# Kernel optimization log

Measured on AMD Instinct MI355X. Metric: run time of the kernel, lower is better.

## Reference

```python
import jax, jax.numpy as jnp
import numpy as np

K = 10        # neighbors kept (after dropping self)
N_SEEDS = 20  # FPS seeds
H = 0.01      # repulsion bandwidth


def setup_inputs() -> dict:
    key = jax.random.key(0)
    pcs = jax.random.uniform(key, (16, 65536, 3), dtype=jnp.float32)
    return {"pcs": pcs}


def farthest_point_sample(xyz, npoint, key):
    """Iterative FPS. xyz: [B,N,C] -> centroids [B,npoint] (int)."""
    B, N, C = xyz.shape
    distance = jnp.full((B, N), 1e10, dtype=xyz.dtype)
    farthest = jax.random.randint(key, (B,), 0, N)
    bidx = jnp.arange(B)

    def step(carry, _):
        dist_min, far = carry
        centroid = xyz[bidx, far][:, None, :]              # [B,1,C]
        d = jnp.sum((xyz - centroid) ** 2, axis=-1)        # [B,N]
        dist_min = jnp.minimum(dist_min, d)
        return (dist_min, jnp.argmax(dist_min, axis=-1)), far

    _, cents = jax.lax.scan(step, (distance, farthest), None, length=npoint)
    return cents.T  # [B, npoint]


def reference(pcs):
    B, N, C = pcs.shape
    seeds = farthest_point_sample(pcs, N_SEEDS, jax.random.key(1))   # [B,S]
    seeds_value = jnp.take_along_axis(
        pcs, jnp.broadcast_to(seeds[:, :, None], (B, N_SEEDS, C)), axis=1
    )  # [B,S,3]
    diff = pcs[:, :, None, :] - seeds_value[:, None, :, :]           # [B,N,S,3]
    sq = jnp.sum(diff * diff, axis=-1)                               # [B,N,S]
    # safe L2 norm (exact zeros at seed-vs-itself)
    dist = jnp.where(sq == 0, 0.0, jnp.sqrt(jnp.where(sq == 0, 1.0, sq)))
    dist_sn = dist.transpose(0, 2, 1)                                # [B,S,N]
    # k+1 smallest distances per seed, ascending (torch.topk largest=False)
    neg_top, _ = jax.lax.top_k(-dist_sn, K + 1)                      # [B,S,K+1]
    top_dist_net = -neg_top[:, :, 1:]                                # drop self, [B,S,K]
    weights = jnp.exp(-(top_dist_net ** 2) / (H * H))
    repulsion = -top_dist_net * weights
    return repulsion.sum(axis=2).sum(axis=1).mean()
```

## Files before the change

kernel.cpp:

```cpp
#include <hip/hip_runtime.h>
#include <cstdint>
#include <cfloat>
#include <cmath>

#define NPTS 65536
#define NB 16
#define NS 20
#define KK 10
#define FPB 16
#define NSm1 (NS - 1)

struct InitIdx { int idx[NB]; };

static __device__ __forceinline__ unsigned long long
agent_ld(const unsigned long long* p) {
    return __hip_atomic_load(p, __ATOMIC_RELAXED, __HIP_MEMORY_SCOPE_AGENT);
}
static __device__ __forceinline__ unsigned int
agent_ld32(const unsigned int* p) {
    return __hip_atomic_load(p, __ATOMIC_RELAXED, __HIP_MEMORY_SCOPE_AGENT);
}

#define INS11(L, SQ)                                                     \
    {                                                                    \
        _Pragma("unroll")                                                \
        for (int jj = 10; jj >= 1; --jj)                                 \
            L[jj] = __builtin_amdgcn_fmed3f(L[jj - 1], L[jj], (SQ));     \
        L[0] = fminf(L[0], (SQ));                                        \
    }

__global__ __launch_bounds__(1024, 4) void fps_kernel(const float* __restrict__ pcs,
                                                      unsigned long long* __restrict__ fkey,
                                                      unsigned int* __restrict__ part,
                                                      float* __restrict__ out,
                                                      InitIdx init) {
    const int u   = blockIdx.x;
    const int xcd = u & 7;
    const int k   = u >> 3;
    const int b   = 2 * xcd + (k >> 4);
    const int j   = k & 15;
    const int t   = threadIdx.x;
    const int lane = t & 63;
    const int w    = t >> 6;
    const float* __restrict__ base = pcs + (size_t)b * NPTS * 3;
    const int pbase = j * 4096 + t * 4;

    const float4* q4 = reinterpret_cast<const float4*>(base + (size_t)pbase * 3);
    float4 A = q4[0], Bv = q4[1], Cv = q4[2];
    float x[4] = { A.x, A.w, Bv.z, Cv.y };
    float y[4] = { A.y, Bv.x, Bv.w, Cv.z };
    float z[4] = { A.z, Bv.y, Cv.x, Cv.w };
    float dm[4] = { 1e10f, 1e10f, 1e10f, 1e10f };

    __shared__ float s_val[16];
    __shared__ int   s_idx[16];
    __shared__ int   s_far;
    __shared__ int   s_seeds[NS];
    __shared__ float xs[4096];
    __shared__ float ys[4096];
    __shared__ float zs[4096];

    int far = init.idx[b];

    for (int s = 0; s < NS; ++s) {
        if (t == 0) s_seeds[s] = far;
        if (s == NSm1) break;

        const float* c = base + (size_t)far * 3;
        const float cx = c[0], cy = c[1], cz = c[2];

        float bestv = -1.0f;
        int   besti = 0;
#pragma unroll
        for (int q = 0; q < 4; ++q) {
            float dx = __fsub_rn(x[q], cx);
            float dy = __fsub_rn(y[q], cy);
            float dz = __fsub_rn(z[q], cz);
            float d  = __fadd_rn(__fadd_rn(__fmul_rn(dx, dx), __fmul_rn(dy, dy)),
                                 __fmul_rn(dz, dz));
            dm[q] = fminf(dm[q], d);
            if (dm[q] > bestv) { bestv = dm[q]; besti = pbase + q; }
        }
#pragma unroll
        for (int off = 32; off >= 1; off >>= 1) {
            float ov = __shfl_down(bestv, off);
            int   oi = __shfl_down(besti, off);
            if (ov > bestv || (ov == bestv && oi < besti)) { bestv = ov; besti = oi; }
        }
        if (lane == 0) { s_val[w] = bestv; s_idx[w] = besti; }
        __syncthreads();

        if (w == 0) {
            unsigned long long kv = 0ULL;
            if (lane < 16) {
                kv = ((unsigned long long)__float_as_uint(s_val[lane]) << 32) |
                     (unsigned long long)(0xFFFFFFFFu - (unsigned int)s_idx[lane]);
            }
#pragma unroll
            for (int off = 8; off >= 1; off >>= 1) {
                unsigned int lo = (unsigned int)kv, hi = (unsigned int)(kv >> 32);
                unsigned int olo = (unsigned int)__shfl_xor((int)lo, off);
                unsigned int ohi = (unsigned int)__shfl_xor((int)hi, off);
                unsigned long long o = ((unsigned long long)ohi << 32) | olo;
                if (o > kv) kv = o;
            }
            unsigned long long* fp = fkey + (size_t)(b * NS + s) * FPB;
            if (lane == 0)
                __hip_atomic_store(&fp[j], kv, __ATOMIC_RELAXED,
                                   __HIP_MEMORY_SCOPE_AGENT);

            const unsigned long long* sl = fp + (lane & 15);
            unsigned long long p0 = agent_ld(sl);
            unsigned long long p1 = agent_ld(sl);
            unsigned long long p2 = agent_ld(sl);
            unsigned long long v;
            for (;;) {
                if (!__any(p0 == 0ULL)) { v = p0; break; }
                p0 = agent_ld(sl);
                if (!__any(p1 == 0ULL)) { v = p1; break; }
                p1 = agent_ld(sl);
                if (!__any(p2 == 0ULL)) { v = p2; break; }
                p2 = agent_ld(sl);
            }
#pragma unroll
            for (int off = 32; off >= 1; off >>= 1) {
                unsigned int lo = (unsigned int)v, hi = (unsigned int)(v >> 32);
                unsigned int olo = (unsigned int)__shfl_xor((int)lo, off);
                unsigned int ohi = (unsigned int)__shfl_xor((int)hi, off);
                unsigned long long o = ((unsigned long long)ohi << 32) | olo;
                if (o > v) v = o;
            }
            if (lane == 0)
                s_far = (int)(0xFFFFFFFFu - (unsigned int)(v & 0xFFFFFFFFull));
        }
        __syncthreads();
        far = s_far;
    }

    {
        float4* xv = reinterpret_cast<float4*>(xs);
        float4* yv = reinterpret_cast<float4*>(ys);
        float4* zv = reinterpret_cast<float4*>(zs);
        xv[t] = make_float4(x[0], x[1], x[2], x[3]);
        yv[t] = make_float4(y[0], y[1], y[2], y[3]);
        zv[t] = make_float4(z[0], z[1], z[2], z[3]);
    }
    __syncthreads();

#pragma unroll
    for (int pass = 0; pass < 2; ++pass) {
        const int s2 = w + pass * 16;
        if (s2 >= NS) break;
        const int sidx = s_seeds[s2];
        const float ccx = base[(size_t)sidx * 3 + 0];
        const float ccy = base[(size_t)sidx * 3 + 1];
        const float ccz = base[(size_t)sidx * 3 + 2];

        float lst[11];
#pragma unroll
        for (int jj = 0; jj < 11; ++jj) lst[jj] = FLT_MAX;

        const float4* xv = reinterpret_cast<const float4*>(xs);
        const float4* yv = reinterpret_cast<const float4*>(ys);
        const float4* zv = reinterpret_cast<const float4*>(zs);
        for (int i = 0; i < 16; ++i) {
            const int p4 = i * 64 + lane;
            float4 qx = xv[p4], qy = yv[p4], qz = zv[p4];
            float px[4] = { qx.x, qx.y, qx.z, qx.w };
            float py[4] = { qy.x, qy.y, qy.z, qy.w };
            float pz[4] = { qz.x, qz.y, qz.z, qz.w };
#pragma unroll
            for (int q = 0; q < 4; ++q) {
                float dx = __fsub_rn(px[q], ccx);
                float dy = __fsub_rn(py[q], ccy);
                float dz = __fsub_rn(pz[q], ccz);
                float sq = __fadd_rn(__fadd_rn(__fmul_rn(dx, dx), __fmul_rn(dy, dy)),
                                     __fmul_rn(dz, dz));
                INS11(lst, sq);
            }
        }
        unsigned int* pr = part + ((size_t)(b * NS + s2) * FPB + j) * 11;
        for (int r = 0; r < 11; ++r) {
            float v = lst[0];
#pragma unroll
            for (int off = 32; off >= 1; off >>= 1) v = fminf(v, __shfl_xor(v, off));
            unsigned long long m = __ballot(lst[0] == v);
            if (lane == (int)__ffsll(m) - 1) {
#pragma unroll
                for (int jj = 0; jj < 10; ++jj) lst[jj] = lst[jj + 1];
                lst[10] = FLT_MAX;
            }
            if (lane == 0)
                __hip_atomic_store(&pr[r], __float_as_uint(v) + 1u,
                                   __ATOMIC_RELAXED, __HIP_MEMORY_SCOPE_AGENT);
        }
    }

    for (int s2 = j; s2 < NS; s2 += FPB) {
        if (w == 0) {
            const unsigned int* sl2 = part + (size_t)(b * NS + s2) * FPB * 11;
            unsigned int k0 = 0, k1 = 0, k2 = (lane + 128 < 176) ? 0u : 1u;
            do {
                if (k0 == 0) k0 = agent_ld32(&sl2[lane]);
                if (k1 == 0) k1 = agent_ld32(&sl2[lane + 64]);
                if (k2 == 0) k2 = agent_ld32(&sl2[lane + 128]);
            } while (__any(k0 == 0 || k1 == 0 || k2 == 0));
            float a0 = __uint_as_float(k0 - 1u);
            float a1 = __uint_as_float(k1 - 1u);
            float a2 = (lane + 128 < 176) ? __uint_as_float(k2 - 1u) : FLT_MAX;

            const float HH = (float)(0.01 * 0.01);
            float acc = 0.0f;
#pragma unroll
            for (int r = 0; r < 11; ++r) {
                float mymin = fminf(a0, fminf(a1, a2));
                float v = mymin;
#pragma unroll
                for (int off = 32; off >= 1; off >>= 1) v = fminf(v, __shfl_xor(v, off));
                unsigned long long m = __ballot(mymin == v);
                if (lane == (int)__ffsll(m) - 1) {
                    if (a0 == v)      a0 = FLT_MAX;
                    else if (a1 == v) a1 = FLT_MAX;
                    else              a2 = FLT_MAX;
                }
                if (lane == 0 && r >= 1) {
                    float sq = v;
                    float dd = (sq == 0.0f) ? 0.0f : __fsqrt_rn(sq);
                    float q2 = __fmul_rn(dd, dd);
                    float wt = expf(__fdiv_rn(-q2, HH));
                    acc = __fadd_rn(acc, -__fmul_rn(dd, wt));
                }
            }
            if (lane == 0) atomicAdd(out, acc * 0.0625f);
        }
    }
}

static inline uint32_t rotl32(uint32_t x, uint32_t d) { return (x << d) | (x >> (32 - d)); }

static void tf2x32(uint32_t k0, uint32_t k1, uint32_t x0, uint32_t x1,
                   uint32_t& y0, uint32_t& y1) {
    const uint32_t ks[3] = { k0, k1, k0 ^ k1 ^ 0x1BD11BDAu };
    const uint32_t rotA[4] = { 13, 15, 26, 6 };
    const uint32_t rotB[4] = { 17, 29, 16, 24 };
    uint32_t v0 = x0 + ks[0], v1 = x1 + ks[1];
    for (int i = 0; i < 5; ++i) {
        const uint32_t* rot = (i % 2 == 0) ? rotA : rotB;
        for (int j = 0; j < 4; ++j) {
            v0 += v1;
            v1 = rotl32(v1, rot[j]);
            v1 ^= v0;
        }
        v0 += ks[(i + 1) % 3];
        v1 += ks[(i + 2) % 3] + (uint32_t)(i + 1);
    }
    y0 = v0; y1 = v1;
}

extern "C" void kernel_launch(void* const* d_in, const int* in_sizes, int n_in,
                              void* d_out, int out_size, void* d_ws, size_t ws_size,
                              hipStream_t stream) {
    const float* pcs = (const float*)d_in[0];
    float* out = (float*)d_out;

    unsigned long long* fkey = (unsigned long long*)((char*)d_ws + 2048);
    unsigned int* part       = (unsigned int*)((char*)d_ws + 49152);

    uint32_t k2_0, k2_1;
    tf2x32(0u, 1u, 0u, 1u, k2_0, k2_1);
    InitIdx init;
    for (int i = 0; i < NB; ++i) {
        uint32_t y0, y1;
        tf2x32(k2_0, k2_1, 0u, (uint32_t)i, y0, y1);
        init.idx[i] = (int)((y0 ^ y1) & 0xFFFFu);
    }

    hipMemsetAsync((char*)d_ws + 2048, 0, 272384, stream);
    hipMemsetAsync(d_out, 0, sizeof(float), stream);

    hipLaunchKernelGGL(fps_kernel, dim3(NB * FPB), dim3(1024), 0, stream,
                       pcs, fkey, part, out, init);
}
```

Baseline: 73.00 us.

## Overlap per-seed kNN scan with FPS global reduction using idle warps

The per-seed nearest-neighbour scan now runs inside the FPS loop. Warp 0 does the cross-block argmax handshake while warps 1-15 each scan a 69-float4 slice of the block's points against the seed just chosen. Their partial top-11 lists go into a shared s_part array, and a final pass merges the 15 partials per seed before the global write. This hides the kNN work behind the FPS synchronisation latency, at the cost of more shared memory and an extra merge step.

```diff
diff --git a/kernel.cpp b/kernel.cpp
--- a/kernel.cpp
+++ b/kernel.cpp
@@ -9,6 +9,7 @@
 #define KK 10
 #define FPB 16
 #define NSm1 (NS - 1)
+#define SPW 69
 
 struct InitIdx { int idx[NB]; };
 
@@ -59,83 +60,7 @@
     __shared__ float xs[4096];
     __shared__ float ys[4096];
     __shared__ float zs[4096];
-
-    int far = init.idx[b];
-
-    for (int s = 0; s < NS; ++s) {
-        if (t == 0) s_seeds[s] = far;
-        if (s == NSm1) break;
-
-        const float* c = base + (size_t)far * 3;
-        const float cx = c[0], cy = c[1], cz = c[2];
-
-        float bestv = -1.0f;
-        int   besti = 0;
-#pragma unroll
-        for (int q = 0; q < 4; ++q) {
-            float dx = __fsub_rn(x[q], cx);
-            float dy = __fsub_rn(y[q], cy);
-            float dz = __fsub_rn(z[q], cz);
-            float d  = __fadd_rn(__fadd_rn(__fmul_rn(dx, dx), __fmul_rn(dy, dy)),
-                                 __fmul_rn(dz, dz));
-            dm[q] = fminf(dm[q], d);
-            if (dm[q] > bestv) { bestv = dm[q]; besti = pbase + q; }
-        }
-#pragma unroll
-        for (int off = 32; off >= 1; off >>= 1) {
-            float ov = __shfl_down(bestv, off);
-            int   oi = __shfl_down(besti, off);
-            if (ov > bestv || (ov == bestv && oi < besti)) { bestv = ov; besti = oi; }
-        }
-        if (lane == 0) { s_val[w] = bestv; s_idx[w] = besti; }
-        __syncthreads();
-
-        if (w == 0) {
-            unsigned long long kv = 0ULL;
-            if (lane < 16) {
-                kv = ((unsigned long long)__float_as_uint(s_val[lane]) << 32) |
-                     (unsigned long long)(0xFFFFFFFFu - (unsigned int)s_idx[lane]);
-            }
-#pragma unroll
-            for (int off = 8; off >= 1; off >>= 1) {
-                unsigned int lo = (unsigned int)kv, hi = (unsigned int)(kv >> 32);
-                unsigned int olo = (unsigned int)__shfl_xor((int)lo, off);
-                unsigned int ohi = (unsigned int)__shfl_xor((int)hi, off);
-                unsigned long long o = ((unsigned long long)ohi << 32) | olo;
-                if (o > kv) kv = o;
-            }
-            unsigned long long* fp = fkey + (size_t)(b * NS + s) * FPB;
-            if (lane == 0)
-                __hip_atomic_store(&fp[j], kv, __ATOMIC_RELAXED,
-                                   __HIP_MEMORY_SCOPE_AGENT);
-
-            const unsigned long long* sl = fp + (lane & 15);
-            unsigned long long p0 = agent_ld(sl);
-            unsigned long long p1 = agent_ld(sl);
-            unsigned long long p2 = agent_ld(sl);
-            unsigned long long v;
-            for (;;) {
-                if (!__any(p0 == 0ULL)) { v = p0; break; }
-                p0 = agent_ld(sl);
-                if (!__any(p1 == 0ULL)) { v = p1; break; }
-                p1 = agent_ld(sl);
-                if (!__any(p2 == 0ULL)) { v = p2; break; }
-                p2 = agent_ld(sl);
-            }
-#pragma unroll
-            for (int off = 32; off >= 1; off >>= 1) {
-                unsigned int lo = (unsigned int)v, hi = (unsigned int)(v >> 32);
-                unsigned int olo = (unsigned int)__shfl_xor((int)lo, off);
-                unsigned int ohi = (unsigned int)__shfl_xor((int)hi, off);
-                unsigned long long o = ((unsigned long long)ohi << 32) | olo;
-                if (o > v) v = o;
-            }
-            if (lane == 0)
-                s_far = (int)(0xFFFFFFFFu - (unsigned int)(v & 0xFFFFFFFFull));
-        }
-        __syncthreads();
-        far = s_far;
-    }
+    __shared__ float s_part[NS][15][11];
 
     {
         float4* xv = reinterpret_cast<float4*>(xs);
@@ -145,50 +70,154 @@
         yv[t] = make_float4(y[0], y[1], y[2], y[3]);
         zv[t] = make_float4(z[0], z[1], z[2], z[3]);
     }
-    __syncthreads();
+
+    int far = init.idx[b];
+
+    for (int s = 0; s < NS; ++s) {
+        if (t == 0) s_seeds[s] = far;
+
+        if (s < NSm1) {
+            const float* c = base + (size_t)far * 3;
+            const float cx = c[0], cy = c[1], cz = c[2];
+
+            float bestv = -1.0f;
+            int   besti = 0;
+#pragma unroll
+            for (int q = 0; q < 4; ++q) {
+                float dx = __fsub_rn(x[q], cx);
+                float dy = __fsub_rn(y[q], cy);
+                float dz = __fsub_rn(z[q], cz);
+                float d  = __fadd_rn(__fadd_rn(__fmul_rn(dx, dx), __fmul_rn(dy, dy)),
+                                     __fmul_rn(dz, dz));
+                dm[q] = fminf(dm[q], d);
+                if (dm[q] > bestv) { bestv = dm[q]; besti = pbase + q; }
+            }
+#pragma unroll
+            for (int off = 32; off >= 1; off >>= 1) {
+                float ov = __shfl_down(bestv, off);
+                int   oi = __shfl_down(besti, off);
+                if (ov > bestv || (ov == bestv && oi < besti)) { bestv = ov; besti = oi; }
+            }
+            if (lane == 0) { s_val[w] = bestv; s_idx[w] = besti; }
+        }
+        __syncthreads();
+
+        if (w == 0) {
+            if (s < NSm1) {
+                unsigned long long kv = 0ULL;
+                if (lane < 16) {
+                    kv = ((unsigned long long)__float_as_uint(s_val[lane]) << 32) |
+                         (unsigned long long)(0xFFFFFFFFu - (unsigned int)s_idx[lane]);
+                }
+#pragma unroll
+                for (int off = 8; off >= 1; off >>= 1) {
+                    unsigned int lo = (unsigned int)kv, hi = (unsigned int)(kv >> 32);
+                    unsigned int olo = (unsigned int)__shfl_xor((int)lo, off);
+                    unsigned int ohi = (unsigned int)__shfl_xor((int)hi, off);
+                    unsigned long long o = ((unsigned long long)ohi << 32) | olo;
+                    if (o > kv) kv = o;
+                }
+                unsigned long long* fp = fkey + (size_t)(b * NS + s) * FPB;
+                if (lane == 0)
+                    __hip_atomic_store(&fp[j], kv, __ATOMIC_RELAXED,
+                                       __HIP_MEMORY_SCOPE_AGENT);
+
+                const unsigned long long* sl = fp + (lane & 15);
+                unsigned long long p0 = agent_ld(sl);
+                unsigned long long p1 = agent_ld(sl);
+                unsigned long long p2 = agent_ld(sl);
+                unsigned long long v;
+                for (;;) {
+                    if (!__any(p0 == 0ULL)) { v = p0; break; }
+                    p0 = agent_ld(sl);
+                    if (!__any(p1 == 0ULL)) { v = p1; break; }
+                    p1 = agent_ld(sl);
+                    if (!__any(p2 == 0ULL)) { v = p2; break; }
+                    p2 = agent_ld(sl);
+                }
+#pragma unroll
+                for (int off = 32; off >= 1; off >>= 1) {
+                    unsigned int lo = (unsigned int)v, hi = (unsigned int)(v >> 32);
+                    unsigned int olo = (unsigned int)__shfl_xor((int)lo, off);
+                    unsigned int ohi = (unsigned int)__shfl_xor((int)hi, off);
+                    unsigned long long o = ((unsigned long long)ohi << 32) | olo;
+                    if (o > v) v = o;
+                }
+                if (lane == 0)
+                    s_far = (int)(0xFFFFFFFFu - (unsigned int)(v & 0xFFFFFFFFull));
+            }
+        } else {
+            const int sidx = s_seeds[s];
+            const float ccx = base[(size_t)sidx * 3 + 0];
+            const float ccy = base[(size_t)sidx * 3 + 1];
+            const float ccz = base[(size_t)sidx * 3 + 2];
+
+            float lst[11];
+#pragma unroll
+            for (int jj = 0; jj < 11; ++jj) lst[jj] = FLT_MAX;
+
+            const int Astart = (w - 1) * SPW;
+            const int Aend   = (Astart + SPW < 1024) ? Astart + SPW : 1024;
+            const float4* xv = reinterpret_cast<const float4*>(xs);
+            const float4* yv = reinterpret_cast<const float4*>(ys);
+            const float4* zv = reinterpret_cast<const float4*>(zs);
+#pragma unroll
+            for (int it = 0; it < 2; ++it) {
+                const int p4 = Astart + it * 64 + lane;
+                if (p4 < Aend) {
+                    float4 qx = xv[p4], qy = yv[p4], qz = zv[p4];
+                    float px[4] = { qx.x, qx.y, qx.z, qx.w };
+                    float py[4] = { qy.x, qy.y, qy.z, qy.w };
+                    float pz[4] = { qz.x, qz.y, qz.z, qz.w };
+#pragma unroll
+                    for (int q = 0; q < 4; ++q) {
+                        float dx = __fsub_rn(px[q], ccx);
+                        float dy = __fsub_rn(py[q], ccy);
+                        float dz = __fsub_rn(pz[q], ccz);
+                        float sq = __fadd_rn(__fadd_rn(__fmul_rn(dx, dx),
+                                                       __fmul_rn(dy, dy)),
+                                             __fmul_rn(dz, dz));
+                        INS11(lst, sq);
+                    }
+                }
+            }
+            float* dst = &s_part[s][w - 1][0];
+            for (int r = 0; r < 11; ++r) {
+                float v = lst[0];
+#pragma unroll
+                for (int off = 32; off >= 1; off >>= 1) v = fminf(v, __shfl_xor(v, off));
+                unsigned long long m = __ballot(lst[0] == v);
+                if (lane == (int)__ffsll(m) - 1) {
+#pragma unroll
+                    for (int jj = 0; jj < 10; ++jj) lst[jj] = lst[jj + 1];
+                    lst[10] = FLT_MAX;
+                }
+                if (lane == 0) dst[r] = v;
+            }
+        }
+        __syncthreads();
+        if (s < NSm1) far = s_far;
+    }
 
 #pragma unroll
     for (int pass = 0; pass < 2; ++pass) {
         const int s2 = w + pass * 16;
         if (s2 >= NS) break;
-        const int sidx = s_seeds[s2];
-        const float ccx = base[(size_t)sidx * 3 + 0];
-        const float ccy = base[(size_t)sidx * 3 + 1];
-        const float ccz = base[(size_t)sidx * 3 + 2];
-
-        float lst[11];
-#pragma unroll
-        for (int jj = 0; jj < 11; ++jj) lst[jj] = FLT_MAX;
-
-        const float4* xv = reinterpret_cast<const float4*>(xs);
-        const float4* yv = reinterpret_cast<const float4*>(ys);
-        const float4* zv = reinterpret_cast<const float4*>(zs);
-        for (int i = 0; i < 16; ++i) {
-            const int p4 = i * 64 + lane;
-            float4 qx = xv[p4], qy = yv[p4], qz = zv[p4];
-            float px[4] = { qx.x, qx.y, qx.z, qx.w };
-            float py[4] = { qy.x, qy.y, qy.z, qy.w };
-            float pz[4] = { qz.x, qz.y, qz.z, qz.w };
-#pragma unroll
-            for (int q = 0; q < 4; ++q) {
-                float dx = __fsub_rn(px[q], ccx);
-                float dy = __fsub_rn(py[q], ccy);
-                float dz = __fsub_rn(pz[q], ccz);
-                float sq = __fadd_rn(__fadd_rn(__fmul_rn(dx, dx), __fmul_rn(dy, dy)),
-                                     __fmul_rn(dz, dz));
-                INS11(lst, sq);
-            }
-        }
+        const float* flat = &s_part[s2][0][0];
+        float a0 = flat[lane];
+        float a1 = flat[lane + 64];
+        float a2 = (lane + 128 < 165) ? flat[lane + 128] : FLT_MAX;
         unsigned int* pr = part + ((size_t)(b * NS + s2) * FPB + j) * 11;
         for (int r = 0; r < 11; ++r) {
-            float v = lst[0];
+            float mymin = fminf(a0, fminf(a1, a2));
+            float v = mymin;
 #pragma unroll
             for (int off = 32; off >= 1; off >>= 1) v = fminf(v, __shfl_xor(v, off));
-            unsigned long long m = __ballot(lst[0] == v);
+            unsigned long long m = __ballot(mymin == v);
             if (lane == (int)__ffsll(m) - 1) {
-#pragma unroll
-                for (int jj = 0; jj < 10; ++jj) lst[jj] = lst[jj + 1];
-                lst[10] = FLT_MAX;
+                if (a0 == v)      a0 = FLT_MAX;
+                else if (a1 == v) a1 = FLT_MAX;
+                else              a2 = FLT_MAX;
             }
             if (lane == 0)
                 __hip_atomic_store(&pr[r], __float_as_uint(v) + 1u,
```

Result: slower. 131.2 us (+79.7%).
